# Kernel optimization log

Measured on AMD Instinct MI355X. Metric: run time of the kernel, lower is better.

The kernel has to match this reference:

```python
import jax, jax.numpy as jnp
import numpy as np

EPS_BN = 1e-5
EPS_W = 1e-8


def setup_inputs() -> dict:
    key = jax.random.key(0)
    ks = jax.random.split(key, 6)
    B, N, S, D1, D2 = 8, 8192, 2048, 128, 256
    Cin = D1 + D2  # 384
    return {
        "points_position": jax.random.normal(ks[0], (B, 3, N), jnp.float32),
        "sampled_points_position": jax.random.normal(ks[1], (B, 3, S), jnp.float32),
        "skip_points_feature": jax.random.normal(ks[2], (B, D1, N), jnp.float32),
        "sampled_points_feature": jax.random.normal(ks[3], (B, D2, S), jnp.float32),
        "W1": jax.random.normal(ks[4], (256, Cin), jnp.float32) * 0.05,
        "b1": jnp.zeros((256,), jnp.float32),
        "g1": jnp.ones((256,), jnp.float32),
        "beta1": jnp.zeros((256,), jnp.float32),
        "W2": jax.random.normal(ks[5], (128, 256), jnp.float32) * 0.05,
        "b2": jnp.zeros((128,), jnp.float32),
        "g2": jnp.ones((128,), jnp.float32),
        "beta2": jnp.zeros((128,), jnp.float32),
    }


def _bn_relu(x, g, b):
    # train-mode BatchNorm1d over (batch, points) per channel, x: [B,N,C]
    mean = jnp.mean(x, axis=(0, 1), keepdims=True)
    var = jnp.mean(jnp.square(x - mean), axis=(0, 1), keepdims=True)  # biased var
    return jax.nn.relu((x - mean) * jax.lax.rsqrt(var + EPS_BN) * g + b)


def reference(points_position, sampled_points_position, skip_points_feature,
              sampled_points_feature, W1, b1, g1, beta1, W2, b2, g2, beta2):
    pos = points_position.transpose(0, 2, 1)            # [B,N,3]
    spos = sampled_points_position.transpose(0, 2, 1)   # [B,S,3]
    sfeat = sampled_points_feature.transpose(0, 2, 1)   # [B,S,D2]

    # squared pairwise distance [B,N,S]
    d = (jnp.sum(pos * pos, axis=-1, keepdims=True)
         - 2.0 * jnp.einsum("bnc,bsc->bns", pos, spos)
         + jnp.sum(spos * spos, axis=-1)[:, None, :])

    # 3 nearest neighbors (smallest distances)
    neg_d3, idx = jax.lax.top_k(-d, 3)                  # [B,N,3]
    d3 = -neg_d3
    w = 1.0 / (d3 + EPS_W)
    w = w / jnp.sum(w, axis=-1, keepdims=True)          # [B,N,3]

    gathered = jax.vmap(lambda f, i: f[i])(sfeat, idx)  # [B,N,3,D2]
    interp = jnp.einsum("bnk,bnkd->bnd", w, gathered)   # [B,N,D2]

    feat = jnp.concatenate([skip_points_feature.transpose(0, 2, 1), interp], axis=-1)  # [B,N,D1+D2]

    h = _bn_relu(jnp.einsum("bnc,oc->bno", feat, W1) + b1, g1, beta1)  # [B,N,256]
    h = _bn_relu(jnp.einsum("bnc,oc->bno", h, W2) + b2, g2, beta2)     # [B,N,128]
    return h.transpose(0, 2, 1)                          # [B,128,N]
```

## Files before the change

### kernel.cpp

```cpp
#include <hip/hip_runtime.h>

constexpr int BATCH = 8;
constexpr int NPT   = 8192;
constexpr int NSMP  = 2048;
constexpr int D1C   = 128;
constexpr int D2C   = 256;
constexpr int CIN   = 384;
constexpr int C1    = 256;
constexpr int C2    = 128;
constexpr int BN_TOTAL = BATCH * NPT;

constexpr int WM = 128, WN = 64, WK = 32;
constexpr int NRB = BN_TOTAL / WM;

typedef __bf16 bf16x8 __attribute__((ext_vector_type(8)));
typedef short  s16x8  __attribute__((ext_vector_type(8)));
typedef float  f32x4  __attribute__((ext_vector_type(4)));

__device__ __forceinline__ unsigned short f2bf(float x) {
  unsigned u = __builtin_bit_cast(unsigned, x);
  u += 0x7fffu + ((u >> 16) & 1u);
  return (unsigned short)(u >> 16);
}
__device__ __forceinline__ float bf2f(unsigned short h) {
  return __builtin_bit_cast(float, (unsigned)h << 16);
}

__device__ __forceinline__ void gld_lds16(const void* g, void* l) {
  __builtin_amdgcn_global_load_lds(
      (const __attribute__((address_space(1))) void*)g,
      (__attribute__((address_space(3))) void*)l, 16, 0, 0);
}

__global__ void transpose_k(const float* __restrict__ in, float* __restrict__ out,
                            int rows, int cols, long inBatch, long outBatch) {
  __shared__ float tile[32][33];
  const float* inb = in + (size_t)blockIdx.z * inBatch;
  float* outb = out + (size_t)blockIdx.z * outBatch;
  int c0 = blockIdx.x * 32;
  int r0 = blockIdx.y * 32;
  int tx = threadIdx.x, ty = threadIdx.y;
#pragma unroll
  for (int i = 0; i < 32; i += 8) {
    int r = r0 + ty + i;
    tile[ty + i][tx] = inb[(size_t)r * cols + c0 + tx];
  }
  __syncthreads();
#pragma unroll
  for (int i = 0; i < 32; i += 8) {
    int c = c0 + ty + i;
    outb[(size_t)c * rows + r0 + tx] = tile[tx][ty + i];
  }
}

__global__ void skip_to_featB(const float* __restrict__ skip,
                              unsigned short* __restrict__ featB) {
  __shared__ float tile[32][33];
  int b = blockIdx.z;
  int n0 = blockIdx.x * 32;
  int d0 = blockIdx.y * 32;
  int tx = threadIdx.x, ty = threadIdx.y;
#pragma unroll
  for (int i = 0; i < 32; i += 8) {
    tile[ty + i][tx] = skip[((size_t)b * D1C + d0 + ty + i) * NPT + n0 + tx];
  }
  __syncthreads();
#pragma unroll
  for (int i = 0; i < 32; i += 8) {
    int n = n0 + ty + i;
    featB[((size_t)b * NPT + n) * CIN + d0 + tx] = f2bf(tile[tx][ty + i]);
  }
}

__global__ void wprep(const float* __restrict__ W, unsigned short* __restrict__ Wh,
                      int total) {
  int i = blockIdx.x * 256 + threadIdx.x;
  if (i >= total) return;
  Wh[i] = f2bf(W[i]);
}

__global__ void pack_spos(const float* __restrict__ spos, float* __restrict__ sposI,
                          float4* __restrict__ qs4) {
  int g = blockIdx.x * 256 + threadIdx.x;
  int b = g >> 11, s = g & (NSMP - 1);
  const float* sp = spos + (size_t)b * 3 * NSMP;
  float x = sp[s], y = sp[NSMP + s], z = sp[2 * NSMP + s];
  sposI[(size_t)g * 3 + 0] = x;
  sposI[(size_t)g * 3 + 1] = y;
  sposI[(size_t)g * 3 + 2] = z;
  qs4[g] = make_float4(-2.f * x, -2.f * y, -2.f * z,
                       fmaf(x, x, fmaf(y, y, z * z)));
}

constexpr int SEG = NSMP / 4;

__device__ __forceinline__ void ins_med3(float kf, float& k0, float& k1,
                                         float& k2, float& k3) {
  float o0 = k0, o1 = k1, o2 = k2;
  k0 = fminf(kf, o0);
  k1 = __builtin_amdgcn_fmed3f(kf, o0, o1);
  k2 = __builtin_amdgcn_fmed3f(kf, o1, o2);
  k3 = __builtin_amdgcn_fmed3f(kf, o2, k3);
}

__global__ __launch_bounds__(256) void knn_kernel(
    const float* __restrict__ pos,
    const float4* __restrict__ qs4g,
    const float* __restrict__ sposI,
    int* __restrict__ idx_out,
    float* __restrict__ wgt_out,
    int* __restrict__ flag_list,
    int* __restrict__ flag_count) {
  __shared__ float4 qs[NSMP];
  __shared__ float mk[4][4][64];

  int tid = threadIdx.x;
  int wave = tid >> 6, lane = tid & 63;
  int blk = blockIdx.x;
  int b = blk >> 7;
  int n = ((blk & 127) << 6) + lane;

  const float4* src = qs4g + (size_t)b * NSMP;
  for (int t = tid; t < NSMP; t += 256) qs[t] = src[t];
  __syncthreads();

  const float* pb = pos + (size_t)b * 3 * NPT;
  float px = pb[n], py = pb[NPT + n], pz = pb[2 * NPT + n];
  float pp = fmaf(px, px, fmaf(py, py, pz * pz));

  const float INF = __builtin_inff();
  float k0 = INF, k1 = INF, k2 = INF, k3 = INF;

  int s0 = wave * SEG;

#define KNN_STEP(Q, SS)                                                   \
  {                                                                       \
    float d = fmaf(px, (Q).x, fmaf(py, (Q).y, fmaf(pz, (Q).z, (Q).w + pp))); \
    unsigned ki = (__builtin_bit_cast(unsigned, d) & 0xFFFFF800u) |       \
                  (unsigned)(SS);                                         \
    ins_med3(__builtin_bit_cast(float, ki), k0, k1, k2, k3);              \
  }

  for (int t = 0; t < SEG; t += 4) {
    int s = s0 + t;
    float4 qa = qs[s], qb = qs[s + 1], qc = qs[s + 2], qd = qs[s + 3];
    KNN_STEP(qa, s + 0)
    KNN_STEP(qb, s + 1)
    KNN_STEP(qc, s + 2)
    KNN_STEP(qd, s + 3)
  }
#undef KNN_STEP

  mk[wave][0][lane] = k0; mk[wave][1][lane] = k1;
  mk[wave][2][lane] = k2; mk[wave][3][lane] = k3;
  __syncthreads();

  if (tid < 64) {
    float K0 = INF, K1 = INF, K2 = INF, K3 = INF;
#pragma unroll
    for (int w = 0; w < 4; w++)
#pragma unroll
      for (int sl = 0; sl < 4; sl++)
        ins_med3(mk[w][sl][tid], K0, K1, K2, K3);

    int p = blk * 64 + tid;
    int I0 = (int)(__builtin_bit_cast(unsigned, K0) & 0x7FFu);
    int I1 = (int)(__builtin_bit_cast(unsigned, K1) & 0x7FFu);
    int I2 = (int)(__builtin_bit_cast(unsigned, K2) & 0x7FFu);
    float d2m = __builtin_bit_cast(float, __builtin_bit_cast(unsigned, K2) & 0xFFFFF800u);
    float d3m = __builtin_bit_cast(float, __builtin_bit_cast(unsigned, K3) & 0xFFFFF800u);
    bool flag = (d3m - d2m) < 2e-3f * fmaxf(d3m, 0.f) + 1e-5f;
    if (flag) {
      int slot = atomicAdd(flag_count, 1);
      flag_list[slot] = p;
    }
    const float* q = sposI + (size_t)b * 3 * NSMP;
    double pxd = (double)px, pyd = (double)py, pzd = (double)pz;
    double dd[3]; int II[3] = {I0, I1, I2};
#pragma unroll
    for (int k = 0; k < 3; k++) {
      double dx = pxd - (double)q[3 * II[k]];
      double dy = pyd - (double)q[3 * II[k] + 1];
      double dz = pzd - (double)q[3 * II[k] + 2];
      dd[k] = dx * dx + dy * dy + dz * dz;
    }
    double w0 = 1.0 / (dd[0] + 1e-8);
    double w1 = 1.0 / (dd[1] + 1e-8);
    double w2 = 1.0 / (dd[2] + 1e-8);
    double inv = 1.0 / (w0 + w1 + w2);
    size_t o = (size_t)p * 3;
    idx_out[o + 0] = I0; idx_out[o + 1] = I1; idx_out[o + 2] = I2;
    wgt_out[o + 0] = (float)(w0 * inv);
    wgt_out[o + 1] = (float)(w1 * inv);
    wgt_out[o + 2] = (float)(w2 * inv);
  }
}

__device__ __forceinline__ bool dless(double d, int i, double D, int I) {
  return d < D || (d == D && i < I);
}
__device__ __forceinline__ void dins3(double d, int i,
                                      double& b0, double& b1, double& b2,
                                      int& i0, int& i1, int& i2) {
  if (dless(d, i, b2, i2)) {
    if (dless(d, i, b1, i1)) {
      b2 = b1; i2 = i1;
      if (dless(d, i, b0, i0)) { b1 = b0; i1 = i0; b0 = d; i0 = i; }
      else                     { b1 = d; i1 = i; }
    } else { b2 = d; i2 = i; }
  }
}

__global__ __launch_bounds__(256) void knn_fallback(
    const float* __restrict__ pos, const float* __restrict__ sposI,
    const int* __restrict__ flag_list, const int* __restrict__ flag_count,
    int* __restrict__ idx_out, float* __restrict__ wgt_out) {
  int wave = threadIdx.x >> 6, lane = threadIdx.x & 63;
  int gw = blockIdx.x * 4 + wave;
  int cnt = *flag_count;
  for (int t = gw; t < cnt; t += 1024) {
    int p = flag_list[t];
    int b = p >> 13, n = p & (NPT - 1);
    const float* pb = pos + (size_t)b * 3 * NPT;
    double px = (double)pb[n], py = (double)pb[NPT + n], pz = (double)pb[2 * NPT + n];
    const float* q = sposI + (size_t)b * 3 * NSMP;
    double b0 = 1e300, b1 = 1e300, b2 = 1e300;
    int i0 = 0x7FFFFFFF, i1 = 0x7FFFFFFF, i2 = 0x7FFFFFFF;
    for (int s = lane; s < NSMP; s += 64) {
      double dx = px - (double)q[3 * s];
      double dy = py - (double)q[3 * s + 1];
      double dz = pz - (double)q[3 * s + 2];
      double d = dx * dx + dy * dy + dz * dz;
      dins3(d, s, b0, b1, b2, i0, i1, i2);
    }
#pragma unroll
    for (int m = 1; m < 64; m <<= 1) {
      double o0 = __shfl_xor(b0, m, 64), o1 = __shfl_xor(b1, m, 64), o2 = __shfl_xor(b2, m, 64);
      int    j0 = __shfl_xor(i0, m, 64), j1 = __shfl_xor(i1, m, 64), j2 = __shfl_xor(i2, m, 64);
      dins3(o0, j0, b0, b1, b2, i0, i1, i2);
      dins3(o1, j1, b0, b1, b2, i0, i1, i2);
      dins3(o2, j2, b0, b1, b2, i0, i1, i2);
    }
    if (lane == 0) {
      double w0 = 1.0 / (b0 + 1e-8);
      double w1 = 1.0 / (b1 + 1e-8);
      double w2 = 1.0 / (b2 + 1e-8);
      double inv = 1.0 / (w0 + w1 + w2);
      size_t o = (size_t)p * 3;
      idx_out[o + 0] = i0; idx_out[o + 1] = i1; idx_out[o + 2] = i2;
      wgt_out[o + 0] = (float)(w0 * inv);
      wgt_out[o + 1] = (float)(w1 * inv);
      wgt_out[o + 2] = (float)(w2 * inv);
    }
  }
}

__global__ __launch_bounds__(256) void interp_kernel(
    const float* __restrict__ sfeatT,
    const int* __restrict__ idx,
    const float* __restrict__ wgt,
    unsigned short* __restrict__ featB) {
  int p = blockIdx.x;
  int c = threadIdx.x;
  int b = p >> 13;
  size_t o = (size_t)p * 3;
  int i0 = idx[o], i1 = idx[o + 1], i2 = idx[o + 2];
  float w0 = wgt[o], w1 = wgt[o + 1], w2 = wgt[o + 2];
  const float* base = sfeatT + (size_t)b * NSMP * D2C;
  float v = w0 * base[(size_t)i0 * D2C + c]
          + w1 * base[(size_t)i1 * D2C + c]
          + w2 * base[(size_t)i2 * D2C + c];
  featB[(size_t)p * CIN + D1C + c] = f2bf(v);
}

__global__ __launch_bounds__(64) void gemm1_wave(
    const unsigned short* __restrict__ featB,
    const unsigned short* __restrict__ W1h,
    const float* __restrict__ bias,
    unsigned short* __restrict__ Y1,
    float* __restrict__ part_s,
    float* __restrict__ part_q) {
  __shared__ __align__(16) unsigned short As[WM * WK];
  __shared__ __align__(16) unsigned short Bs[WN * WK];
  int lane = threadIdx.x;
  int m16 = lane & 15, quad = lane >> 4;
  int rb = blockIdx.x, cb = blockIdx.y;
  int row0 = rb * WM, col0 = cb * WN;
  int row16 = lane >> 2, col8 = (lane & 3) * 8;

  f32x4 acc[8][4];
#pragma unroll
  for (int j = 0; j < 4; j++) {
    float bj = bias[col0 + j * 16 + m16];
#pragma unroll
    for (int i = 0; i < 8; i++) acc[i][j] = f32x4{bj, bj, bj, bj};
  }

  for (int k0 = 0; k0 < CIN; k0 += WK) {
#pragma unroll
    for (int c = 0; c < 8; c++)
      gld_lds16(&featB[(size_t)(row0 + c * 16 + row16) * CIN + k0 + col8],
                &As[c * 16 * WK]);
#pragma unroll
    for (int c = 0; c < 4; c++)
      gld_lds16(&W1h[(size_t)(col0 + c * 16 + row16) * CIN + k0 + col8],
                &Bs[c * 16 * WK]);
    __syncthreads();

    bf16x8 a[8], bf[4];
#pragma unroll
    for (int i = 0; i < 8; i++)
      a[i] = __builtin_bit_cast(bf16x8, *(const s16x8*)&As[(i * 16 + m16) * WK + quad * 8]);
#pragma unroll
    for (int j = 0; j < 4; j++)
      bf[j] = __builtin_bit_cast(bf16x8, *(const s16x8*)&Bs[(j * 16 + m16) * WK + quad * 8]);
#pragma unroll
    for (int i = 0; i < 8; i++)
#pragma unroll
      for (int j = 0; j < 4; j++)
        acc[i][j] = __builtin_amdgcn_mfma_f32_16x16x32_bf16(a[i], bf[j], acc[i][j], 0, 0, 0);
    __syncthreads();
  }

#pragma unroll
  for (int j = 0; j < 4; j++) {
    int col = col0 + j * 16 + m16;
    float s = 0.f, q = 0.f;
#pragma unroll
    for (int i = 0; i < 8; i++)
#pragma unroll
      for (int r = 0; r < 4; r++) {
        float v = acc[i][j][r];
        Y1[(size_t)(row0 + i * 16 + quad * 4 + r) * C1 + col] = f2bf(v);
        s += v; q = fmaf(v, v, q);
      }
    s += __shfl_xor(s, 16, 64); s += __shfl_xor(s, 32, 64);
    q += __shfl_xor(q, 16, 64); q += __shfl_xor(q, 32, 64);
    if (quad == 0) {
      part_s[(size_t)col * NRB + rb] = s;
      part_q[(size_t)col * NRB + rb] = q;
    }
  }
}

__global__ __launch_bounds__(64) void gemm2_wave(
    const unsigned short* __restrict__ Y1,
    const float* __restrict__ scale1, const float* __restrict__ shift1,
    const unsigned short* __restrict__ W2h,
    const float* __restrict__ bias,
    unsigned short* __restrict__ Y2,
    float* __restrict__ part_s,
    float* __restrict__ part_q) {
  __shared__ __align__(16) unsigned short As[WM * WK];
  __shared__ __align__(16) unsigned short Bs[WN * WK];
  __shared__ float scs[C1], shs[C1];
  int lane = threadIdx.x;
  int m16 = lane & 15, quad = lane >> 4;
  int rb = blockIdx.x, cb = blockIdx.y;
  int row0 = rb * WM, col0 = cb * WN;
  int row16 = lane >> 2, col8 = (lane & 3) * 8;

  for (int t = lane; t < C1; t += 64) { scs[t] = scale1[t]; shs[t] = shift1[t]; }

  f32x4 acc[8][4];
#pragma unroll
  for (int j = 0; j < 4; j++) {
    float bj = bias[col0 + j * 16 + m16];
#pragma unroll
    for (int i = 0; i < 8; i++) acc[i][j] = f32x4{bj, bj, bj, bj};
  }
  __syncthreads();

  for (int k0 = 0; k0 < C1; k0 += WK) {
#pragma unroll
    for (int c = 0; c < 4; c++)
      gld_lds16(&W2h[(size_t)(col0 + c * 16 + row16) * C1 + k0 + col8],
                &Bs[c * 16 * WK]);
#pragma unroll
    for (int c = 0; c < 8; c++) {
      int row = c * 16 + row16;
      s16x8 v = *(const s16x8*)&Y1[(size_t)(row0 + row) * C1 + k0 + col8];
      unsigned short ov[8];
#pragma unroll
      for (int e = 0; e < 8; e++) {
        float x = bf2f((unsigned short)v[e]);
        float y = fmaxf(fmaf(x, scs[k0 + col8 + e], shs[k0 + col8 + e]), 0.f);
        ov[e] = f2bf(y);
      }
      *(s16x8*)&As[row * WK + col8] = *(const s16x8*)ov;
    }
    __syncthreads();

    bf16x8 a[8], bf[4];
#pragma unroll
    for (int i = 0; i < 8; i++)
      a[i] = __builtin_bit_cast(bf16x8, *(const s16x8*)&As[(i * 16 + m16) * WK + quad * 8]);
#pragma unroll
    for (int j = 0; j < 4; j++)
      bf[j] = __builtin_bit_cast(bf16x8, *(const s16x8*)&Bs[(j * 16 + m16) * WK + quad * 8]);
#pragma unroll
    for (int i = 0; i < 8; i++)
#pragma unroll
      for (int j = 0; j < 4; j++)
        acc[i][j] = __builtin_amdgcn_mfma_f32_16x16x32_bf16(a[i], bf[j], acc[i][j], 0, 0, 0);
    __syncthreads();
  }

#pragma unroll
  for (int j = 0; j < 4; j++) {
    int col = col0 + j * 16 + m16;
    float s = 0.f, q = 0.f;
#pragma unroll
    for (int i = 0; i < 8; i++)
#pragma unroll
      for (int r = 0; r < 4; r++) {
        float v = acc[i][j][r];
        Y2[(size_t)(row0 + i * 16 + quad * 4 + r) * C2 + col] = f2bf(v);
        s += v; q = fmaf(v, v, q);
      }
    s += __shfl_xor(s, 16, 64); s += __shfl_xor(s, 32, 64);
    q += __shfl_xor(q, 16, 64); q += __shfl_xor(q, 32, 64);
    if (quad == 0) {
      part_s[(size_t)col * NRB + rb] = s;
      part_q[(size_t)col * NRB + rb] = q;
    }
  }
}

__global__ __launch_bounds__(256) void bn_reduce_coef(
    const float* __restrict__ part_s, const float* __restrict__ part_q, int nrb,
    const float* __restrict__ g, const float* __restrict__ beta,
    float* __restrict__ scale, float* __restrict__ shift) {
  int ch = blockIdx.x;
  int tid = threadIdx.x;
  float s = 0.f, q = 0.f;
  for (int t = tid; t < nrb; t += 256) {
    s += part_s[(size_t)ch * nrb + t];
    q += part_q[(size_t)ch * nrb + t];
  }
#pragma unroll
  for (int m = 1; m < 64; m <<= 1) {
    s += __shfl_xor(s, m, 64);
    q += __shfl_xor(q, m, 64);
  }
  __shared__ float ls[4], lq[4];
  int wave = tid >> 6;
  if ((tid & 63) == 0) { ls[wave] = s; lq[wave] = q; }
  __syncthreads();
  if (tid == 0) {
    s = ls[0] + ls[1] + ls[2] + ls[3];
    q = lq[0] + lq[1] + lq[2] + lq[3];
    const float invBN = 1.0f / (float)BN_TOTAL;
    float mean = s * invBN;
    float var = q * invBN - mean * mean;
    float sc = g[ch] / sqrtf(var + 1e-5f);
    scale[ch] = sc;
    shift[ch] = beta[ch] - mean * sc;
  }
}

__global__ void final_kernel(const unsigned short* __restrict__ Y2,
                             const float* __restrict__ scale, const float* __restrict__ shift,
                             float* __restrict__ out) {
  __shared__ float tile[32][33];
  int b = blockIdx.z;
  int n0 = blockIdx.x * 32;
  int c0 = blockIdx.y * 32;
  int tx = threadIdx.x, ty = threadIdx.y;
  float sc = scale[c0 + tx];
  float sh = shift[c0 + tx];
#pragma unroll
  for (int i = 0; i < 32; i += 8) {
    int n = n0 + ty + i;
    float v = bf2f(Y2[((size_t)b * NPT + n) * C2 + c0 + tx]);
    tile[ty + i][tx] = fmaxf(fmaf(v, sc, sh), 0.f);
  }
  __syncthreads();
#pragma unroll
  for (int i = 0; i < 32; i += 8) {
    int c = c0 + ty + i;
    out[((size_t)b * C2 + c) * NPT + n0 + tx] = tile[tx][ty + i];
  }
}

extern "C" void kernel_launch(void* const* d_in, const int* in_sizes, int n_in,
                              void* d_out, int out_size, void* d_ws, size_t ws_size,
                              hipStream_t stream) {
  (void)in_sizes; (void)n_in; (void)out_size; (void)ws_size;
  const float* pos   = (const float*)d_in[0];
  const float* spos  = (const float*)d_in[1];
  const float* skip  = (const float*)d_in[2];
  const float* sfeat = (const float*)d_in[3];
  const float* W1    = (const float*)d_in[4];
  const float* b1    = (const float*)d_in[5];
  const float* g1    = (const float*)d_in[6];
  const float* beta1 = (const float*)d_in[7];
  const float* W2    = (const float*)d_in[8];
  const float* b2    = (const float*)d_in[9];
  const float* g2    = (const float*)d_in[10];
  const float* beta2 = (const float*)d_in[11];
  float* out = (float*)d_out;

  float* ws = (float*)d_ws;
  size_t off = 0;
  float* sfeatT  = ws + off; off += (size_t)BATCH * NSMP * D2C;
  unsigned short* featB = (unsigned short*)(ws + off); off += (size_t)BN_TOTAL * CIN / 2;
  unsigned short* Y1    = (unsigned short*)(ws + off); off += (size_t)BN_TOTAL * C1 / 2;
  unsigned short* Y2    = (unsigned short*)(ws + off); off += (size_t)BN_TOTAL * C2 / 2;
  unsigned short* W1h   = (unsigned short*)(ws + off); off += (size_t)C1 * CIN / 2;
  unsigned short* W2h   = (unsigned short*)(ws + off); off += (size_t)C2 * C1 / 2;
  int*   knn_idx = (int*)(ws + off); off += (size_t)BN_TOTAL * 3;
  float* knn_w   = ws + off; off += (size_t)BN_TOTAL * 3;
  float* sposI   = ws + off; off += (size_t)BATCH * NSMP * 3;
  float4* qs4    = (float4*)(ws + off); off += (size_t)BATCH * NSMP * 4;
  int* flag_list = (int*)(ws + off); off += (size_t)BN_TOTAL;
  float* part1_s = ws + off; off += (size_t)C1 * NRB;
  float* part1_q = ws + off; off += (size_t)C1 * NRB;
  float* part2_s = ws + off; off += (size_t)C2 * NRB;
  float* part2_q = ws + off; off += (size_t)C2 * NRB;
  float* stats   = ws + off; off += 2048;
  int*   flag_count = (int*)stats;
  float* scale1 = stats + 256, *shift1 = stats + 512;
  float* scale2 = stats + 768, *shift2 = stats + 1024;

  hipMemsetAsync(flag_count, 0, sizeof(int), stream);

  dim3 tb(32, 8);
  transpose_k<<<dim3(NSMP / 32, D2C / 32, BATCH), tb, 0, stream>>>(
      sfeat, sfeatT, D2C, NSMP, (long)D2C * NSMP, (long)NSMP * D2C);
  wprep<<<(C1 * CIN + 255) / 256, 256, 0, stream>>>(W1, W1h, C1 * CIN);
  wprep<<<(C2 * C1 + 255) / 256, 256, 0, stream>>>(W2, W2h, C2 * C1);
  skip_to_featB<<<dim3(NPT / 32, D1C / 32, BATCH), tb, 0, stream>>>(skip, featB);

  pack_spos<<<BATCH * NSMP / 256, 256, 0, stream>>>(spos, sposI, qs4);
  knn_kernel<<<BN_TOTAL / 64, 256, 0, stream>>>(pos, qs4, sposI, knn_idx, knn_w,
                                                flag_list, flag_count);
  knn_fallback<<<256, 256, 0, stream>>>(pos, sposI, flag_list, flag_count,
                                        knn_idx, knn_w);
  interp_kernel<<<BN_TOTAL, 256, 0, stream>>>(sfeatT, knn_idx, knn_w, featB);

  gemm1_wave<<<dim3(NRB, C1 / WN), 64, 0, stream>>>(
      featB, W1h, b1, Y1, part1_s, part1_q);
  bn_reduce_coef<<<C1, 256, 0, stream>>>(part1_s, part1_q, NRB, g1, beta1, scale1, shift1);

  gemm2_wave<<<dim3(NRB, C2 / WN), 64, 0, stream>>>(
      Y1, scale1, shift1, W2h, b2, Y2, part2_s, part2_q);
  bn_reduce_coef<<<C2, 256, 0, stream>>>(part2_s, part2_q, NRB, g2, beta2, scale2, shift2);

  final_kernel<<<dim3(NPT / 32, C2 / 32, BATCH), tb, 0, stream>>>(Y2, scale2, shift2, out);
}
```

Baseline: 301.7 us.

## Process four query points per thread in KNN to reuse LDS sample loads

The KNN kernel now has each thread handle four query points against the same shared-memory sample stream, so each LDS float4 read is amortized over four distance computations. The grid shrinks fourfold, and the final merge is spread across all four waves instead of only one. The per-point |p|^2 term is dropped from the inner loop and added back only in the tie-detection threshold, which removes one add per distance. This costs more registers and gives fewer blocks to hide latency.

```diff
diff --git a/kernel.cpp b/kernel.cpp
--- a/kernel.cpp
+++ b/kernel.cpp
@@ -93,6 +93,7 @@
 }
 
 constexpr int SEG = NSMP / 4;
+constexpr int PPL = 4;
 
 __device__ __forceinline__ void ins_med3(float kf, float& k0, float& k1,
                                          float& k2, float& k3) {
@@ -112,70 +113,80 @@
     int* __restrict__ flag_list,
     int* __restrict__ flag_count) {
   __shared__ float4 qs[NSMP];
-  __shared__ float mk[4][4][64];
+  __shared__ float mk[4][PPL][4][64];
 
   int tid = threadIdx.x;
   int wave = tid >> 6, lane = tid & 63;
   int blk = blockIdx.x;
-  int b = blk >> 7;
-  int n = ((blk & 127) << 6) + lane;
+  int b = blk >> 5;
+  int nbase = ((blk & 31) << 8) + lane;
 
   const float4* src = qs4g + (size_t)b * NSMP;
   for (int t = tid; t < NSMP; t += 256) qs[t] = src[t];
-  __syncthreads();
 
   const float* pb = pos + (size_t)b * 3 * NPT;
-  float px = pb[n], py = pb[NPT + n], pz = pb[2 * NPT + n];
-  float pp = fmaf(px, px, fmaf(py, py, pz * pz));
+  float px[PPL], py[PPL], pz[PPL];
+#pragma unroll
+  for (int p = 0; p < PPL; p++) {
+    int n = nbase + 64 * p;
+    px[p] = pb[n]; py[p] = pb[NPT + n]; pz[p] = pb[2 * NPT + n];
+  }
+  __syncthreads();
 
   const float INF = __builtin_inff();
-  float k0 = INF, k1 = INF, k2 = INF, k3 = INF;
+  float k0[PPL], k1[PPL], k2[PPL], k3[PPL];
+#pragma unroll
+  for (int p = 0; p < PPL; p++) { k0[p] = INF; k1[p] = INF; k2[p] = INF; k3[p] = INF; }
 
   int s0 = wave * SEG;
-
-#define KNN_STEP(Q, SS)                                                   \
-  {                                                                       \
-    float d = fmaf(px, (Q).x, fmaf(py, (Q).y, fmaf(pz, (Q).z, (Q).w + pp))); \
-    unsigned ki = (__builtin_bit_cast(unsigned, d) & 0xFFFFF800u) |       \
-                  (unsigned)(SS);                                         \
-    ins_med3(__builtin_bit_cast(float, ki), k0, k1, k2, k3);              \
-  }
-
   for (int t = 0; t < SEG; t += 4) {
     int s = s0 + t;
-    float4 qa = qs[s], qb = qs[s + 1], qc = qs[s + 2], qd = qs[s + 3];
-    KNN_STEP(qa, s + 0)
-    KNN_STEP(qb, s + 1)
-    KNN_STEP(qc, s + 2)
-    KNN_STEP(qd, s + 3)
-  }
-#undef KNN_STEP
-
-  mk[wave][0][lane] = k0; mk[wave][1][lane] = k1;
-  mk[wave][2][lane] = k2; mk[wave][3][lane] = k3;
-  __syncthreads();
-
-  if (tid < 64) {
+    float4 qq[4] = {qs[s], qs[s + 1], qs[s + 2], qs[s + 3]};
+#pragma unroll
+    for (int u = 0; u < 4; u++) {
+      float4 q = qq[u];
+      unsigned si = (unsigned)(s + u);
+#pragma unroll
+      for (int p = 0; p < PPL; p++) {
+        float d = fmaf(px[p], q.x, fmaf(py[p], q.y, fmaf(pz[p], q.z, q.w)));
+        unsigned ki = (__builtin_bit_cast(unsigned, d) & 0xFFFFF800u) | si;
+        ins_med3(__builtin_bit_cast(float, ki), k0[p], k1[p], k2[p], k3[p]);
+      }
+    }
+  }
+
+#pragma unroll
+  for (int p = 0; p < PPL; p++) {
+    mk[wave][p][0][lane] = k0[p]; mk[wave][p][1][lane] = k1[p];
+    mk[wave][p][2][lane] = k2[p]; mk[wave][p][3][lane] = k3[p];
+  }
+  __syncthreads();
+
+  {
+    int myp = tid >> 6, myl = tid & 63;
     float K0 = INF, K1 = INF, K2 = INF, K3 = INF;
 #pragma unroll
     for (int w = 0; w < 4; w++)
 #pragma unroll
       for (int sl = 0; sl < 4; sl++)
-        ins_med3(mk[w][sl][tid], K0, K1, K2, K3);
-
-    int p = blk * 64 + tid;
+        ins_med3(mk[w][myp][sl][myl], K0, K1, K2, K3);
+
+    float fx = px[myp], fy = py[myp], fz = pz[myp];
+    float pp = fmaf(fx, fx, fmaf(fy, fy, fz * fz));
+
+    int p = blk * 256 + tid;
     int I0 = (int)(__builtin_bit_cast(unsigned, K0) & 0x7FFu);
     int I1 = (int)(__builtin_bit_cast(unsigned, K1) & 0x7FFu);
     int I2 = (int)(__builtin_bit_cast(unsigned, K2) & 0x7FFu);
     float d2m = __builtin_bit_cast(float, __builtin_bit_cast(unsigned, K2) & 0xFFFFF800u);
     float d3m = __builtin_bit_cast(float, __builtin_bit_cast(unsigned, K3) & 0xFFFFF800u);
-    bool flag = (d3m - d2m) < 2e-3f * fmaxf(d3m, 0.f) + 1e-5f;
+    bool flag = (d3m - d2m) < 2e-3f * fmaxf(d3m + pp, 0.f) + 1e-5f;
     if (flag) {
       int slot = atomicAdd(flag_count, 1);
       flag_list[slot] = p;
     }
     const float* q = sposI + (size_t)b * 3 * NSMP;
-    double pxd = (double)px, pyd = (double)py, pzd = (double)pz;
+    double pxd = (double)fx, pyd = (double)fy, pzd = (double)fz;
     double dd[3]; int II[3] = {I0, I1, I2};
 #pragma unroll
     for (int k = 0; k < 3; k++) {
@@ -533,8 +544,8 @@
   skip_to_featB<<<dim3(NPT / 32, D1C / 32, BATCH), tb, 0, stream>>>(skip, featB);
 
   pack_spos<<<BATCH * NSMP / 256, 256, 0, stream>>>(spos, sposI, qs4);
-  knn_kernel<<<BN_TOTAL / 64, 256, 0, stream>>>(pos, qs4, sposI, knn_idx, knn_w,
-                                                flag_list, flag_count);
+  knn_kernel<<<BN_TOTAL / 256, 256, 0, stream>>>(pos, qs4, sposI, knn_idx, knn_w,
+                                                 flag_list, flag_count);
   knn_fallback<<<256, 256, 0, stream>>>(pos, sposI, flag_list, flag_count,
                                         knn_idx, knn_w);
   interp_kernel<<<BN_TOTAL, 256, 0, stream>>>(sfeatT, knn_idx, knn_w, featB);
```

After: 313.7 us. 4.0% more time.
